# Kernel tuning notes

Hardware: AMD Instinct MI355X
Metric: run time of the kernel (lower is better)

The kernel has to match this reference:

```python
import jax, jax.numpy as jnp
import numpy as np

N = 50000
E = 600000
IN_DIM = 256
H1, H2, H3 = 128, 64, 64
HEADS = 8


def _add_self_loops(edge_index, edge_weight=None):
    loop = jnp.arange(N, dtype=edge_index.dtype)
    src = jnp.concatenate([edge_index[0], loop])
    dst = jnp.concatenate([edge_index[1], loop])
    if edge_weight is None:
        return src, dst, None
    ew = jnp.concatenate([edge_weight, jnp.ones((N,), edge_weight.dtype)])
    return src, dst, ew


def gcn_conv(x, edge_index, edge_weight, W, b):
    # PyG GCNConv: add self-loops (weight 1), symmetric normalization, scatter-add.
    src, dst, ew = _add_self_loops(edge_index, edge_weight)
    deg = jax.ops.segment_sum(ew, dst, num_segments=N)          # [N]
    dinv = jnp.where(deg > 0, jax.lax.rsqrt(jnp.maximum(deg, 1e-12)), 0.0)
    coeff = dinv[src] * ew * dinv[dst]                          # [E+N]
    h = x @ W                                                    # [N, out]
    out = jax.ops.segment_sum(coeff[:, None] * h[src], dst, num_segments=N)
    return out + b


def gat_conv(x, edge_index, W, att_src, att_dst, b):
    # PyG GATConv, heads=HEADS, concat=False (mean over heads), leaky_relu slope 0.2.
    src, dst, _ = _add_self_loops(edge_index)
    C = W.shape[1] // HEADS
    h = (x @ W).reshape(N, HEADS, C)                             # [N,H,C]
    a_s = jnp.sum(h * att_src, axis=-1)                          # [N,H]
    a_d = jnp.sum(h * att_dst, axis=-1)                          # [N,H]
    e = jax.nn.leaky_relu(a_s[src] + a_d[dst], negative_slope=0.2)  # [E',H]
    # scatter-softmax over edges sharing a destination
    m = jax.ops.segment_max(e, dst, num_segments=N)              # [N,H]
    p = jnp.exp(e - m[dst])
    s = jax.ops.segment_sum(p, dst, num_segments=N)              # [N,H]
    alpha = p / (s[dst] + 1e-16)                                 # [E',H]
    out = jax.ops.segment_sum(alpha[:, :, None] * h[src], dst, num_segments=N)  # [N,H,C]
    return jnp.mean(out, axis=1) + b


def setup_inputs() -> dict:
    key = jax.random.key(0)
    ks = jax.random.split(key, 12)
    x = jax.random.normal(ks[0], (N, IN_DIM), dtype=jnp.float32)
    edge_index = jax.random.randint(ks[1], (2, E), 0, N, dtype=jnp.int32)
    edge_weight = jax.random.uniform(ks[2], (E,), dtype=jnp.float32)
    def glorot(k, shape):
        fan = shape[0] + shape[-1]
        return jax.random.normal(k, shape, dtype=jnp.float32) * np.sqrt(2.0 / fan)
    return {
        "x": x, "edge_index": edge_index, "edge_weight": edge_weight,
        "gc1_w": glorot(ks[3], (IN_DIM, H1)), "gc1_b": jnp.zeros((H1,), jnp.float32),
        "gat_w": glorot(ks[4], (H1, HEADS * H2)),
        "att_src": glorot(ks[5], (HEADS, H2)), "att_dst": glorot(ks[6], (HEADS, H2)),
        "gat_b": jnp.zeros((H2,), jnp.float32),
        "gc2_w": glorot(ks[7], (H2, H3)), "gc2_b": jnp.zeros((H3,), jnp.float32),
        "fc_w": glorot(ks[8], (H3, 1)), "fc_b": jnp.zeros((1,), jnp.float32),
    }


def reference(x, edge_index, edge_weight, gc1_w, gc1_b, gat_w, att_src, att_dst,
              gat_b, gc2_w, gc2_b, fc_w, fc_b):
    # dropout is inference no-op
    h = jax.nn.relu(gcn_conv(x, edge_index, edge_weight, gc1_w, gc1_b))
    h = jax.nn.relu(gat_conv(h, edge_index, gat_w, att_src, att_dst, gat_b))
    h = jax.nn.relu(gcn_conv(h, edge_index, edge_weight, gc2_w, gc2_b))
    return h @ fc_w + fc_b                                       # [N,1]
```

## Files before the change

### kernel.cpp

```cpp
#include <hip/hip_runtime.h>
#include <hip/hip_bf16.h>

#define GNN_N 50000
#define GNN_E 600000

typedef unsigned int uint;
typedef unsigned short ushort;
using short8 = __attribute__((ext_vector_type(8))) short;
using f32x4  = __attribute__((ext_vector_type(4))) float;
using f32x2  = __attribute__((ext_vector_type(2))) float;

__device__ __forceinline__ float leaky02(float x) { return x > 0.f ? x : 0.2f * x; }
__device__ __forceinline__ ushort f2b(float f) {
    uint u = __float_as_uint(f);
    return (ushort)((u + 0x7fffu + ((u >> 16) & 1u)) >> 16);
}
__device__ __forceinline__ float b2f(ushort b) { return __uint_as_float(((uint)b) << 16); }
__device__ __forceinline__ float blo(uint u) { return __uint_as_float(u << 16); }
__device__ __forceinline__ float bhi(uint u) { return __uint_as_float(u & 0xffff0000u); }

__device__ __forceinline__ void pkfma(f32x2& d, f32x2 a, f32x2 b) {
    asm("v_pk_fma_f32 %0, %1, %2, %0" : "+v"(d) : "v"(a), "v"(b));
}
__device__ __forceinline__ f32x2 shfl2(f32x2 x, int srcLane) {
    union { f32x2 f; long long l; } u;
    u.f = x;
    u.l = __shfl(u.l, srcLane);
    return u.f;
}
__device__ __forceinline__ f32x2 shflx2(f32x2 x, int m) {
    union { f32x2 f; long long l; } u;
    u.f = x;
    u.l = __shfl_xor(u.l, m);
    return u.f;
}

__global__ void gnn_hist(const int* __restrict__ dst, int* __restrict__ cnt, int e) {
    int i = blockIdx.x * blockDim.x + threadIdx.x;
    if (i < e) atomicAdd(&cnt[dst[i]], 1);
}
__global__ void gnn_scan1(const int* __restrict__ cnt, int* __restrict__ row_ptr,
                          int* __restrict__ blksum, int n) {
    __shared__ int sh[256];
    int tid = threadIdx.x;
    int base = blockIdx.x * 1024 + tid * 4;
    int v0 = (base + 0 < n) ? cnt[base + 0] : 0;
    int v1 = (base + 1 < n) ? cnt[base + 1] : 0;
    int v2 = (base + 2 < n) ? cnt[base + 2] : 0;
    int v3 = (base + 3 < n) ? cnt[base + 3] : 0;
    int tsum = v0 + v1 + v2 + v3;
    sh[tid] = tsum;
    __syncthreads();
    for (int off = 1; off < 256; off <<= 1) {
        int t = (tid >= off) ? sh[tid - off] : 0;
        __syncthreads();
        sh[tid] += t;
        __syncthreads();
    }
    int excl = sh[tid] - tsum;
    if (base + 0 < n) row_ptr[base + 0] = excl; excl += v0;
    if (base + 1 < n) row_ptr[base + 1] = excl; excl += v1;
    if (base + 2 < n) row_ptr[base + 2] = excl; excl += v2;
    if (base + 3 < n) row_ptr[base + 3] = excl;
    if (tid == 255) blksum[blockIdx.x] = sh[255];
}
__global__ void gnn_scan2(int* blksum, int nblk, int* row_ptr_end, int total) {
    if (threadIdx.x == 0 && blockIdx.x == 0) {
        int run = 0;
        for (int b = 0; b < nblk; ++b) { int t = blksum[b]; blksum[b] = run; run += t; }
        *row_ptr_end = total;
    }
}
__global__ void gnn_scan3(int* row_ptr, const int* __restrict__ blksum, int n) {
    int i = blockIdx.x * blockDim.x + threadIdx.x;
    if (i < n) row_ptr[i] += blksum[i >> 10];
}
__global__ void gnn_scatter_idx(const int* __restrict__ dst, const int* __restrict__ row_ptr,
                                int* __restrict__ fill, int* __restrict__ tord, int e) {
    int i = blockIdx.x * blockDim.x + threadIdx.x;
    if (i >= e) return;
    int d = dst[i];
    int pos = row_ptr[d] + atomicAdd(&fill[d], 1);
    tord[pos] = i;
}
__global__ __launch_bounds__(256) void gnn_sortdeg(const float* __restrict__ ew,
                                                   int* __restrict__ tord,
                                                   const int* __restrict__ row_ptr,
                                                   float* __restrict__ dinv, int n) {
    int v = blockIdx.x * 4 + (threadIdx.x >> 6);
    int lane = threadIdx.x & 63;
    if (v >= n) return;
    int beg = row_ptr[v], end = row_ptr[v + 1];
    int cnt = end - beg;
    if (cnt <= 64) {
        int val = (lane < cnt) ? tord[beg + lane] : 0x7fffffff;
#pragma unroll
        for (int k = 2; k <= 64; k <<= 1) {
#pragma unroll
            for (int j = k >> 1; j >= 1; j >>= 1) {
                int other = __shfl_xor(val, j);
                bool keepMin = (((lane & j) == 0) == ((lane & k) == 0));
                val = keepMin ? min(val, other) : max(val, other);
            }
        }
        if (lane < cnt) tord[beg + lane] = val;
        float s = (lane < cnt) ? ew[val] : 0.f;
#pragma unroll
        for (int m = 32; m; m >>= 1) s += __shfl_xor(s, m);
        if (lane == 0) dinv[v] = rsqrtf(1.0f + s);
    } else {
        if (lane == 0) {
            for (int i = beg + 1; i < end; ++i) {
                int key = tord[i];
                int k2 = i - 1;
                while (k2 >= beg && tord[k2] > key) { tord[k2 + 1] = tord[k2]; --k2; }
                tord[k2 + 1] = key;
            }
            float s = 1.f;
            for (int i = beg; i < end; ++i) s += ew[tord[i]];
            dinv[v] = rsqrtf(s);
        }
    }
}
__global__ void gnn_edgefin(const int* __restrict__ src, const int* __restrict__ dst,
                            const float* __restrict__ ew, const float* __restrict__ dinv,
                            const int* __restrict__ tord, int* __restrict__ esrc,
                            float* __restrict__ ecw, int e) {
    int pos = blockIdx.x * blockDim.x + threadIdx.x;
    if (pos >= e) return;
    int i = tord[pos];
    int s = src[i];
    esrc[pos] = s;
    ecw[pos] = dinv[s] * ew[i] * dinv[dst[i]];
}

__global__ void gnn_prep(const float* __restrict__ gc1_w, const float* __restrict__ gat_w,
                         const float* __restrict__ gc2_w, const float* __restrict__ att_src,
                         const float* __restrict__ att_dst, ushort* __restrict__ w1t,
                         ushort* __restrict__ w2s_t, ushort* __restrict__ w3t,
                         float* __restrict__ wa_t) {
    int t = blockIdx.x * 256 + threadIdx.x;
    if (t < 32768) {
        int k = t >> 7, n = t & 127;
        w1t[n * 256 + k] = f2b(gc1_w[t]);
        return;
    }
    t -= 32768;
    if (t < 65536) {
        int c = t >> 10, r = t & 1023;
        int h = r >> 7, k = r & 127;
        w2s_t[t] = f2b(0.125f * gat_w[(size_t)k * 512 + h * 64 + c]);
        return;
    }
    t -= 65536;
    if (t < 4096) {
        int k = t >> 6, n = t & 63;
        w3t[n * 64 + k] = f2b(gc2_w[t]);
        return;
    }
    t -= 4096;
    if (t < 2048) {
        int j = t >> 7, k = t & 127;
        int h = j & 7;
        const float* av = (j < 8) ? att_src : att_dst;
        float s = 0.f;
        for (int c = 0; c < 64; ++c) s += gat_w[(size_t)k * 512 + h * 64 + c] * av[h * 64 + c];
        wa_t[j * 128 + k] = s;
    }
}

template <bool AF32, bool BIAS>
__global__ __launch_bounds__(256) void gnn_mfma_gemm(const void* __restrict__ Av,
                                                     const ushort* __restrict__ Bt,
                                                     ushort* __restrict__ C,
                                                     const float* __restrict__ bias,
                                                     int M, int N, int K) {
    __shared__ ushort As[64 * 40];
    __shared__ ushort Bs[64 * 40];
    const int tid = threadIdx.x;
    const int wv = tid >> 6, lane = tid & 63;
    const int g = lane >> 4, r = lane & 15;
    const int brow = blockIdx.y << 6, bcol = blockIdx.x << 6;

    const int srow = tid >> 2;
    const int skoff = (tid & 3) << 3;
    int arow = brow + srow;
    if (arow >= M) arow = M - 1;
    const ushort* A16 = (const ushort*)Av;
    const float*  A32 = (const float*)Av;
    const ushort* Ap16 = A16 + (size_t)arow * K + skoff;
    const float*  Ap32 = A32 + (size_t)arow * K + skoff;
    const ushort* Bp = Bt + (size_t)(bcol + srow) * K + skoff;
    ushort* AsW = &As[srow * 40 + skoff];
    ushort* BsW = &Bs[srow * 40 + skoff];

    f32x4 acc[4] = {};

    for (int k0 = 0; k0 < K; k0 += 32) {
        if constexpr (AF32) {
            float4 f0 = *(const float4*)(Ap32 + k0);
            float4 f1 = *(const float4*)(Ap32 + k0 + 4);
            short8 t;
            t[0] = (short)f2b(f0.x); t[1] = (short)f2b(f0.y);
            t[2] = (short)f2b(f0.z); t[3] = (short)f2b(f0.w);
            t[4] = (short)f2b(f1.x); t[5] = (short)f2b(f1.y);
            t[6] = (short)f2b(f1.z); t[7] = (short)f2b(f1.w);
            *(short8*)AsW = t;
        } else {
            *(short8*)AsW = *(const short8*)(Ap16 + k0);
        }
        *(short8*)BsW = *(const short8*)(Bp + k0);
        __syncthreads();
        short8 bfrag = *(const short8*)&Bs[(wv * 16 + r) * 40 + g * 8];
#pragma unroll
        for (int mb = 0; mb < 4; ++mb) {
            short8 afrag = *(const short8*)&As[(mb * 16 + r) * 40 + g * 8];
            acc[mb] = __builtin_amdgcn_mfma_f32_16x16x32_bf16(afrag, bfrag, acc[mb], 0, 0, 0);
        }
        __syncthreads();
    }

    const int col = bcol + wv * 16 + r;
    float bv = 0.f;
    if constexpr (BIAS) bv = bias[col];
#pragma unroll
    for (int mb = 0; mb < 4; ++mb) {
        int rowb = brow + mb * 16 + g * 4;
#pragma unroll
        for (int rr = 0; rr < 4; ++rr) {
            int row = rowb + rr;
            if (row < M) {
                float val = acc[mb][rr];
                if constexpr (BIAS) {
                    val += bv;
                    val = val > 0.f ? val : 0.f;
                }
                C[(size_t)row * N + col] = f2b(val);
            }
        }
    }
}

__global__ __launch_bounds__(256) void gnn_gcn_node128_asd(const int* __restrict__ row_ptr,
                                                           const int* __restrict__ esrc,
                                                           const float* __restrict__ ecw,
                                                           const float* __restrict__ dinv,
                                                           const ushort* __restrict__ hb,
                                                           const float* __restrict__ b,
                                                           const float* __restrict__ wa,
                                                           ushort* __restrict__ out,
                                                           float* __restrict__ a_s,
                                                           float* __restrict__ a_d, int n) {
    __shared__ float swa[16 * 128];
    for (int i = threadIdx.x; i < 16 * 128; i += 256) swa[i] = wa[i];
    __syncthreads();
    int v = blockIdx.x * 4 + (threadIdx.x >> 6);
    int lane = threadIdx.x & 63;
    if (v >= n) return;
    const int sl = lane & 31;
    const int half = lane >> 5;
    float di = dinv[v];
    float a0, a1, a2, a3;
    {
        float scl = half ? 0.f : di * di;
        uint2 u = *(const uint2*)(hb + (size_t)v * 128 + 4 * sl);
        a0 = scl * blo(u.x); a1 = scl * bhi(u.x);
        a2 = scl * blo(u.y); a3 = scl * bhi(u.y);
    }
    int beg = row_ptr[v], end = row_ptr[v + 1];
    int cntE = end - beg;
    int pairs = cntE >> 1;
    int i = 0;
    for (; i + 4 <= pairs; i += 4) {
        int s[4]; float c[4]; uint2 u[4];
#pragma unroll
        for (int t = 0; t < 4; ++t) s[t] = esrc[beg + 2 * (i + t) + half];
#pragma unroll
        for (int t = 0; t < 4; ++t) c[t] = ecw[beg + 2 * (i + t) + half];
#pragma unroll
        for (int t = 0; t < 4; ++t) u[t] = *(const uint2*)(hb + (size_t)s[t] * 128 + 4 * sl);
#pragma unroll
        for (int t = 0; t < 4; ++t) {
            a0 += c[t] * blo(u[t].x); a1 += c[t] * bhi(u[t].x);
            a2 += c[t] * blo(u[t].y); a3 += c[t] * bhi(u[t].y);
        }
    }
    for (; i < pairs; ++i) {
        int s = esrc[beg + 2 * i + half];
        float c = ecw[beg + 2 * i + half];
        uint2 u = *(const uint2*)(hb + (size_t)s * 128 + 4 * sl);
        a0 += c * blo(u.x); a1 += c * bhi(u.x);
        a2 += c * blo(u.y); a3 += c * bhi(u.y);
    }
    if (cntE & 1) {
        int s = esrc[end - 1];
        float c = half ? 0.f : ecw[end - 1];
        uint2 u = *(const uint2*)(hb + (size_t)s * 128 + 4 * sl);
        a0 += c * blo(u.x); a1 += c * bhi(u.x);
        a2 += c * blo(u.y); a3 += c * bhi(u.y);
    }
    a0 += __shfl_xor(a0, 32); a1 += __shfl_xor(a1, 32);
    a2 += __shfl_xor(a2, 32); a3 += __shfl_xor(a3, 32);

    float4 bv = *(const float4*)(b + 4 * sl);
    float o0 = a0 + bv.x, o1 = a1 + bv.y, o2 = a2 + bv.z, o3 = a3 + bv.w;
    o0 = o0 > 0.f ? o0 : 0.f; o1 = o1 > 0.f ? o1 : 0.f;
    o2 = o2 > 0.f ? o2 : 0.f; o3 = o3 > 0.f ? o3 : 0.f;
    if (lane < 32) {
        uint2 w;
        w.x = (uint)f2b(o0) | ((uint)f2b(o1) << 16);
        w.y = (uint)f2b(o2) | ((uint)f2b(o3) << 16);
        *(uint2*)(out + (size_t)v * 128 + 4 * sl) = w;
    }

    float part[16];
#pragma unroll
    for (int j = 0; j < 16; ++j) {
        const float* wj = &swa[j * 128 + 4 * sl];
        part[j] = o0 * wj[0] + o1 * wj[1] + o2 * wj[2] + o3 * wj[3];
    }
#pragma unroll
    for (int m = 1; m < 32; m <<= 1) {
#pragma unroll
        for (int j = 0; j < 16; ++j) part[j] += __shfl_xor(part[j], m);
    }
    if (lane == 0) {
#pragma unroll
        for (int j = 0; j < 8; ++j) {
            a_s[(size_t)v * 8 + j] = part[j];
            a_d[(size_t)v * 8 + j] = part[8 + j];
        }
    }
}

__global__ __launch_bounds__(256) void gnn_gat_z(const int* __restrict__ row_ptr,
                                                 const int* __restrict__ esrc,
                                                 const float* __restrict__ a_s,
                                                 const float* __restrict__ a_d,
                                                 const ushort* __restrict__ g1b,
                                                 ushort* __restrict__ zb, int n) {
    int v = blockIdx.x * 4 + (threadIdx.x >> 6);
    int lane = threadIdx.x & 63;
    if (v >= n) return;
    const int sl = lane & 31;
    const int half = lane >> 5;
    const int hh = lane & 7;
    const int hbase = lane & 32;
    const float adh = a_d[(size_t)v * 8 + hh];

    f32x2 zA[8] = {}, zB[8] = {};
    float sloc = 0.f;
    {
        float pv = __expf(leaky02(a_s[(size_t)v * 8 + hh] + adh));
        if (half) pv = 0.f;
        sloc += pv;
        f32x2 pv2; pv2[0] = pv; pv2[1] = pv;
        uint2 u = *(const uint2*)(g1b + (size_t)v * 128 + 4 * sl);
        f32x2 gA; gA[0] = blo(u.x); gA[1] = bhi(u.x);
        f32x2 gB; gB[0] = blo(u.y); gB[1] = bhi(u.y);
#pragma unroll
        for (int h = 0; h < 8; ++h) {
            f32x2 ph2 = shfl2(pv2, hbase | h);
            pkfma(zA[h], gA, ph2);
            pkfma(zB[h], gB, ph2);
        }
    }
    int beg = row_ptr[v], end = row_ptr[v + 1];
    int cntE = end - beg;
    int pairs = cntE >> 1;
    int i = 0;
    for (; i + 2 <= pairs; i += 2) {
        int s[2]; float e[2]; uint2 u[2];
#pragma unroll
        for (int t = 0; t < 2; ++t) s[t] = esrc[beg + 2 * (i + t) + half];
#pragma unroll
        for (int t = 0; t < 2; ++t) e[t] = a_s[(size_t)s[t] * 8 + hh];
#pragma unroll
        for (int t = 0; t < 2; ++t) u[t] = *(const uint2*)(g1b + (size_t)s[t] * 128 + 4 * sl);
#pragma unroll
        for (int t = 0; t < 2; ++t) {
            float pv = __expf(leaky02(e[t] + adh));
            sloc += pv;
            f32x2 pv2; pv2[0] = pv; pv2[1] = pv;
            f32x2 gA; gA[0] = blo(u[t].x); gA[1] = bhi(u[t].x);
            f32x2 gB; gB[0] = blo(u[t].y); gB[1] = bhi(u[t].y);
#pragma unroll
            for (int h = 0; h < 8; ++h) {
                f32x2 ph2 = shfl2(pv2, hbase | h);
                pkfma(zA[h], gA, ph2);
                pkfma(zB[h], gB, ph2);
            }
        }
    }
    for (; i < pairs; ++i) {
        int s = esrc[beg + 2 * i + half];
        float pv = __expf(leaky02(a_s[(size_t)s * 8 + hh] + adh));
        sloc += pv;
        f32x2 pv2; pv2[0] = pv; pv2[1] = pv;
        uint2 u = *(const uint2*)(g1b + (size_t)s * 128 + 4 * sl);
        f32x2 gA; gA[0] = blo(u.x); gA[1] = bhi(u.x);
        f32x2 gB; gB[0] = blo(u.y); gB[1] = bhi(u.y);
#pragma unroll
        for (int h = 0; h < 8; ++h) {
            f32x2 ph2 = shfl2(pv2, hbase | h);
            pkfma(zA[h], gA, ph2);
            pkfma(zB[h], gB, ph2);
        }
    }
    if (cntE & 1) {
        int s = esrc[end - 1];
        float pv = __expf(leaky02(a_s[(size_t)s * 8 + hh] + adh));
        if (half) pv = 0.f;
        sloc += pv;
        f32x2 pv2; pv2[0] = pv; pv2[1] = pv;
        uint2 u = *(const uint2*)(g1b + (size_t)s * 128 + 4 * sl);
        f32x2 gA; gA[0] = blo(u.x); gA[1] = bhi(u.x);
        f32x2 gB; gB[0] = blo(u.y); gB[1] = bhi(u.y);
#pragma unroll
        for (int h = 0; h < 8; ++h) {
            f32x2 ph2 = shfl2(pv2, hbase | h);
            pkfma(zA[h], gA, ph2);
            pkfma(zB[h], gB, ph2);
        }
    }
    float slx = sloc + __shfl_xor(sloc, 32) + 1e-16f;
#pragma unroll
    for (int h = 0; h < 8; ++h) {
        zA[h] = zA[h] + shflx2(zA[h], 32);
        zB[h] = zB[h] + shflx2(zB[h], 32);
    }
    if (lane < 32) {
#pragma unroll
        for (int h = 0; h < 8; ++h) {
            float rs = 1.f / __shfl(slx, h);
            uint2 w;
            w.x = (uint)f2b(zA[h][0] * rs) | ((uint)f2b(zA[h][1] * rs) << 16);
            w.y = (uint)f2b(zB[h][0] * rs) | ((uint)f2b(zB[h][1] * rs) << 16);
            *(uint2*)(zb + (size_t)v * 1024 + h * 128 + 4 * sl) = w;
        }
    }
}

__global__ __launch_bounds__(256) void gnn_gcn_node64_fc(const int* __restrict__ row_ptr,
                                                         const int* __restrict__ esrc,
                                                         const float* __restrict__ ecw,
                                                         const float* __restrict__ dinv,
                                                         const ushort* __restrict__ hb,
                                                         const float* __restrict__ b,
                                                         const float* __restrict__ fc_w,
                                                         const float* __restrict__ fc_b,
                                                         float* __restrict__ out, int n) {
    int v = blockIdx.x * 4 + (threadIdx.x >> 6);
    int lane = threadIdx.x & 63;
    if (v >= n) return;
    const int sl = lane & 31;
    const int half = lane >> 5;
    float di = dinv[v];
    float a0, a1;
    {
        float scl = half ? 0.f : di * di;
        uint u = *(const uint*)(hb + (size_t)v * 64 + 2 * sl);
        a0 = scl * blo(u); a1 = scl * bhi(u);
    }
    int beg = row_ptr[v], end = row_ptr[v + 1];
    int cntE = end - beg;
    int pairs = cntE >> 1;
    int i = 0;
    for (; i + 4 <= pairs; i += 4) {
        int s[4]; float c[4]; uint u[4];
#pragma unroll
        for (int t = 0; t < 4; ++t) s[t] = esrc[beg + 2 * (i + t) + half];
#pragma unroll
        for (int t = 0; t < 4; ++t) c[t] = ecw[beg + 2 * (i + t) + half];
#pragma unroll
        for (int t = 0; t < 4; ++t) u[t] = *(const uint*)(hb + (size_t)s[t] * 64 + 2 * sl);
#pragma unroll
        for (int t = 0; t < 4; ++t) { a0 += c[t] * blo(u[t]); a1 += c[t] * bhi(u[t]); }
    }
    for (; i < pairs; ++i) {
        int s = esrc[beg + 2 * i + half];
        float c = ecw[beg + 2 * i + half];
        uint u = *(const uint*)(hb + (size_t)s * 64 + 2 * sl);
        a0 += c * blo(u); a1 += c * bhi(u);
    }
    if (cntE & 1) {
        int s = esrc[end - 1];
        float c = half ? 0.f : ecw[end - 1];
        uint u = *(const uint*)(hb + (size_t)s * 64 + 2 * sl);
        a0 += c * blo(u); a1 += c * bhi(u);
    }
    a0 += __shfl_xor(a0, 32);
    a1 += __shfl_xor(a1, 32);
    float o0 = a0 + b[2 * sl];
    float o1 = a1 + b[2 * sl + 1];
    o0 = o0 > 0.f ? o0 : 0.f;
    o1 = o1 > 0.f ? o1 : 0.f;
    float val = o0 * fc_w[2 * sl] + o1 * fc_w[2 * sl + 1];
#pragma unroll
    for (int m = 1; m < 32; m <<= 1) val += __shfl_xor(val, m);
    if (lane == 0) out[v] = val + fc_b[0];
}

extern "C" void kernel_launch(void* const* d_in, const int* in_sizes, int n_in,
                              void* d_out, int out_size, void* d_ws, size_t ws_size,
                              hipStream_t stream) {
    const float* x       = (const float*)d_in[0];
    const int*   ei      = (const int*)d_in[1];
    const float* ew      = (const float*)d_in[2];
    const float* gc1_w   = (const float*)d_in[3];
    const float* gc1_b   = (const float*)d_in[4];
    const float* gat_w   = (const float*)d_in[5];
    const float* att_src = (const float*)d_in[6];
    const float* att_dst = (const float*)d_in[7];
    const float* gat_b   = (const float*)d_in[8];
    const float* gc2_w   = (const float*)d_in[9];
    const float* gc2_b   = (const float*)d_in[10];
    const float* fc_w    = (const float*)d_in[11];
    const float* fc_b    = (const float*)d_in[12];
    float* out = (float*)d_out;

    const int N = GNN_N;
    const int E = in_sizes[2];
    const int* src = ei;
    const int* dst = ei + E;

    char* p = (char*)d_ws;
    ushort* zb  = (ushort*)p; p += (size_t)N * 1024 * 2;
    ushort* h1b = (ushort*)p; p += (size_t)N * 128 * 2;
    ushort* g1b = (ushort*)p; p += (size_t)N * 128 * 2;
    ushort* g2b = (ushort*)p; p += (size_t)N * 64 * 2;
    ushort* h3b = (ushort*)p; p += (size_t)N * 64 * 2;
    ushort* w1t = (ushort*)p; p += (size_t)128 * 256 * 2;
    ushort* w2s_t = (ushort*)p; p += (size_t)64 * 1024 * 2;
    ushort* w3t = (ushort*)p; p += (size_t)64 * 64 * 2;
    float*  wa_t = (float*)p; p += 16 * 128 * 4;
    float*  a_s = (float*)p;  p += (size_t)N * 8 * 4;
    float*  a_d = (float*)p;  p += (size_t)N * 8 * 4;
    int* row_ptr = (int*)p;   p += (size_t)(N + 64) * 4;
    int* esrc = (int*)p;      p += (size_t)E * 4;
    float* ecw = (float*)p;   p += (size_t)E * 4;
    int* tord = (int*)p;      p += (size_t)E * 4;
    int* cnt = (int*)p;       p += (size_t)N * 4;
    int* fill = (int*)p;      p += (size_t)N * 4;
    float* dinv = (float*)p;  p += (size_t)N * 4;
    int* blksum = (int*)p;    p += 4096;

    auto cdiv = [](long a, long b) { return (int)((a + b - 1) / b); };

    hipMemsetAsync(cnt, 0, (size_t)N * 8, stream);
    gnn_hist<<<cdiv(E, 256), 256, 0, stream>>>(dst, cnt, E);
    const int nblk = cdiv(N, 1024);
    gnn_scan1<<<nblk, 256, 0, stream>>>(cnt, row_ptr, blksum, N);
    gnn_scan2<<<1, 64, 0, stream>>>(blksum, nblk, row_ptr + N, E);
    gnn_scan3<<<cdiv(N, 256), 256, 0, stream>>>(row_ptr, blksum, N);
    gnn_scatter_idx<<<cdiv(E, 256), 256, 0, stream>>>(dst, row_ptr, fill, tord, E);
    gnn_sortdeg<<<cdiv(N, 4), 256, 0, stream>>>(ew, tord, row_ptr, dinv, N);
    gnn_edgefin<<<cdiv(E, 256), 256, 0, stream>>>(src, dst, ew, dinv, tord, esrc, ecw, E);

    gnn_prep<<<408, 256, 0, stream>>>(gc1_w, gat_w, gc2_w, att_src, att_dst, w1t, w2s_t, w3t, wa_t);

    {
        dim3 grid(128 / 64, cdiv(N, 64));
        gnn_mfma_gemm<true, false><<<grid, 256, 0, stream>>>(x, w1t, h1b, nullptr, N, 128, 256);
    }
    gnn_gcn_node128_asd<<<cdiv(N, 4), 256, 0, stream>>>(row_ptr, esrc, ecw, dinv, h1b, gc1_b,
                                                        wa_t, g1b, a_s, a_d, N);

    gnn_gat_z<<<cdiv(N, 4), 256, 0, stream>>>(row_ptr, esrc, a_s, a_d, g1b, zb, N);
    {
        dim3 grid(1, cdiv(N, 64));
        gnn_mfma_gemm<false, true><<<grid, 256, 0, stream>>>(zb, w2s_t, g2b, gat_b, N, 64, 1024);
    }

    {
        dim3 grid(1, cdiv(N, 64));
        gnn_mfma_gemm<false, false><<<grid, 256, 0, stream>>>(g2b, w3t, h3b, nullptr, N, 64, 64);
    }
    gnn_gcn_node64_fc<<<cdiv(N, 4), 256, 0, stream>>>(row_ptr, esrc, ecw, dinv, h3b, gc2_b,
                                                      fc_w, fc_b, out, N);
}
```

Measured before the change: 337.6 us.

## Split each node's edge aggregation across two wavefronts with LDS reduction

The three per-node aggregation kernels (GCN layer 1, GAT softmax-weighted sum, GCN layer 2 with FC) now give each destination node two 64-lane wavefronts instead of one. Each wave handles alternating edge pairs, and the partial sums are combined through shared memory behind a block barrier. This shortens the serial per-node edge loop and raises memory-level parallelism on the gathers. The costs are twice as many blocks, an added __syncthreads, an LDS round trip, and the second wave sitting idle during the epilogue; the GAT kernel also needs about 8KB of shared memory per block to exchange its z partials.

New measurement: 407.2 us. 20.6% more time.

```diff
diff --git a/kernel.cpp b/kernel.cpp
--- a/kernel.cpp
+++ b/kernel.cpp
@@ -252,83 +252,100 @@
                                                            float* __restrict__ a_s,
                                                            float* __restrict__ a_d, int n) {
     __shared__ float swa[16 * 128];
+    __shared__ float psh[2][128];
     for (int i = threadIdx.x; i < 16 * 128; i += 256) swa[i] = wa[i];
-    __syncthreads();
-    int v = blockIdx.x * 4 + (threadIdx.x >> 6);
-    int lane = threadIdx.x & 63;
-    if (v >= n) return;
+    const int tid = threadIdx.x;
+    const int node_i = tid >> 7;
+    const int nw = (tid >> 6) & 1;
+    const int lane = tid & 63;
+    const int v = blockIdx.x * 2 + node_i;
+    const bool active = v < n;
     const int sl = lane & 31;
     const int half = lane >> 5;
-    float di = dinv[v];
-    float a0, a1, a2, a3;
-    {
-        float scl = half ? 0.f : di * di;
+
+    float a0 = 0.f, a1 = 0.f, a2 = 0.f, a3 = 0.f;
+    int beg = 0, end = 0;
+    if (active) { beg = row_ptr[v]; end = row_ptr[v + 1]; }
+    int cntE = end - beg;
+    int pairs = cntE >> 1;
+
+    if (active && nw == 0) {
+        float scl = half ? 0.f : dinv[v] * dinv[v];
         uint2 u = *(const uint2*)(hb + (size_t)v * 128 + 4 * sl);
         a0 = scl * blo(u.x); a1 = scl * bhi(u.x);
         a2 = scl * blo(u.y); a3 = scl * bhi(u.y);
     }
-    int beg = row_ptr[v], end = row_ptr[v + 1];
-    int cntE = end - beg;
-    int pairs = cntE >> 1;
-    int i = 0;
-    for (; i + 4 <= pairs; i += 4) {
-        int s[4]; float c[4]; uint2 u[4];
-#pragma unroll
-        for (int t = 0; t < 4; ++t) s[t] = esrc[beg + 2 * (i + t) + half];
-#pragma unroll
-        for (int t = 0; t < 4; ++t) c[t] = ecw[beg + 2 * (i + t) + half];
-#pragma unroll
-        for (int t = 0; t < 4; ++t) u[t] = *(const uint2*)(hb + (size_t)s[t] * 128 + 4 * sl);
-#pragma unroll
-        for (int t = 0; t < 4; ++t) {
-            a0 += c[t] * blo(u[t].x); a1 += c[t] * bhi(u[t].x);
-            a2 += c[t] * blo(u[t].y); a3 += c[t] * bhi(u[t].y);
-        }
-    }
-    for (; i < pairs; ++i) {
-        int s = esrc[beg + 2 * i + half];
-        float c = ecw[beg + 2 * i + half];
-        uint2 u = *(const uint2*)(hb + (size_t)s * 128 + 4 * sl);
-        a0 += c * blo(u.x); a1 += c * bhi(u.x);
-        a2 += c * blo(u.y); a3 += c * bhi(u.y);
-    }
-    if (cntE & 1) {
-        int s = esrc[end - 1];
-        float c = half ? 0.f : ecw[end - 1];
-        uint2 u = *(const uint2*)(hb + (size_t)s * 128 + 4 * sl);
-        a0 += c * blo(u.x); a1 += c * bhi(u.x);
-        a2 += c * blo(u.y); a3 += c * bhi(u.y);
+    if (active) {
+        int i = nw;
+        for (; i + 2 < pairs; i += 4) {
+            int pa = beg + 2 * i + half;
+            int pb = beg + 2 * (i + 2) + half;
+            int s0 = esrc[pa], s1 = esrc[pb];
+            float c0 = ecw[pa], c1 = ecw[pb];
+            uint2 u0 = *(const uint2*)(hb + (size_t)s0 * 128 + 4 * sl);
+            uint2 u1 = *(const uint2*)(hb + (size_t)s1 * 128 + 4 * sl);
+            a0 += c0 * blo(u0.x); a1 += c0 * bhi(u0.x);
+            a2 += c0 * blo(u0.y); a3 += c0 * bhi(u0.y);
+            a0 += c1 * blo(u1.x); a1 += c1 * bhi(u1.x);
+            a2 += c1 * blo(u1.y); a3 += c1 * bhi(u1.y);
+        }
+        for (; i < pairs; i += 2) {
+            int pa = beg + 2 * i + half;
+            int s0 = esrc[pa];
+            float c0 = ecw[pa];
+            uint2 u0 = *(const uint2*)(hb + (size_t)s0 * 128 + 4 * sl);
+            a0 += c0 * blo(u0.x); a1 += c0 * bhi(u0.x);
+            a2 += c0 * blo(u0.y); a3 += c0 * bhi(u0.y);
+        }
+        if (nw == 0 && (cntE & 1)) {
+            int s = esrc[end - 1];
+            float c = half ? 0.f : ecw[end - 1];
+            uint2 u = *(const uint2*)(hb + (size_t)s * 128 + 4 * sl);
+            a0 += c * blo(u.x); a1 += c * bhi(u.x);
+            a2 += c * blo(u.y); a3 += c * bhi(u.y);
+        }
     }
     a0 += __shfl_xor(a0, 32); a1 += __shfl_xor(a1, 32);
     a2 += __shfl_xor(a2, 32); a3 += __shfl_xor(a3, 32);
 
-    float4 bv = *(const float4*)(b + 4 * sl);
-    float o0 = a0 + bv.x, o1 = a1 + bv.y, o2 = a2 + bv.z, o3 = a3 + bv.w;
-    o0 = o0 > 0.f ? o0 : 0.f; o1 = o1 > 0.f ? o1 : 0.f;
-    o2 = o2 > 0.f ? o2 : 0.f; o3 = o3 > 0.f ? o3 : 0.f;
-    if (lane < 32) {
+    if (active && nw == 1 && lane < 32) {
+        psh[node_i][4 * sl + 0] = a0;
+        psh[node_i][4 * sl + 1] = a1;
+        psh[node_i][4 * sl + 2] = a2;
+        psh[node_i][4 * sl + 3] = a3;
+    }
+    __syncthreads();
+    if (active && nw == 0 && lane < 32) {
+        a0 += psh[node_i][4 * sl + 0];
+        a1 += psh[node_i][4 * sl + 1];
+        a2 += psh[node_i][4 * sl + 2];
+        a3 += psh[node_i][4 * sl + 3];
+        float4 bv = *(const float4*)(b + 4 * sl);
+        float o0 = a0 + bv.x, o1 = a1 + bv.y, o2 = a2 + bv.z, o3 = a3 + bv.w;
+        o0 = o0 > 0.f ? o0 : 0.f; o1 = o1 > 0.f ? o1 : 0.f;
+        o2 = o2 > 0.f ? o2 : 0.f; o3 = o3 > 0.f ? o3 : 0.f;
         uint2 w;
         w.x = (uint)f2b(o0) | ((uint)f2b(o1) << 16);
         w.y = (uint)f2b(o2) | ((uint)f2b(o3) << 16);
         *(uint2*)(out + (size_t)v * 128 + 4 * sl) = w;
-    }
-
-    float part[16];
-#pragma unroll
-    for (int j = 0; j < 16; ++j) {
-        const float* wj = &swa[j * 128 + 4 * sl];
-        part[j] = o0 * wj[0] + o1 * wj[1] + o2 * wj[2] + o3 * wj[3];
-    }
-#pragma unroll
-    for (int m = 1; m < 32; m <<= 1) {
-#pragma unroll
-        for (int j = 0; j < 16; ++j) part[j] += __shfl_xor(part[j], m);
-    }
-    if (lane == 0) {
-#pragma unroll
-        for (int j = 0; j < 8; ++j) {
-            a_s[(size_t)v * 8 + j] = part[j];
-            a_d[(size_t)v * 8 + j] = part[8 + j];
+
+        float part[16];
+#pragma unroll
+        for (int j = 0; j < 16; ++j) {
+            const float* wj = &swa[j * 128 + 4 * sl];
+            part[j] = o0 * wj[0] + o1 * wj[1] + o2 * wj[2] + o3 * wj[3];
+        }
+#pragma unroll
+        for (int m = 1; m < 32; m <<= 1) {
+#pragma unroll
+            for (int j = 0; j < 16; ++j) part[j] += __shfl_xor(part[j], m);
+        }
+        if (lane == 0) {
+#pragma unroll
+            for (int j = 0; j < 8; ++j) {
+                a_s[(size_t)v * 8 + j] = part[j];
+                a_d[(size_t)v * 8 + j] = part[8 + j];
+            }
         }
     }
 }
@@ -339,18 +356,30 @@
                                                  const float* __restrict__ a_d,
                                                  const ushort* __restrict__ g1b,
                                                  ushort* __restrict__ zb, int n) {
-    int v = blockIdx.x * 4 + (threadIdx.x >> 6);
-    int lane = threadIdx.x & 63;
-    if (v >= n) return;
+    __shared__ float zsh[2][1032];
+    const int tid = threadIdx.x;
+    const int node_i = tid >> 7;
+    const int nw = (tid >> 6) & 1;
+    const int lane = tid & 63;
+    const int v = blockIdx.x * 2 + node_i;
+    const bool active = v < n;
     const int sl = lane & 31;
     const int half = lane >> 5;
     const int hh = lane & 7;
     const int hbase = lane & 32;
-    const float adh = a_d[(size_t)v * 8 + hh];
 
     f32x2 zA[8] = {}, zB[8] = {};
     float sloc = 0.f;
-    {
+    int beg = 0, end = 0;
+    float adh = 0.f;
+    if (active) {
+        beg = row_ptr[v]; end = row_ptr[v + 1];
+        adh = a_d[(size_t)v * 8 + hh];
+    }
+    int cntE = end - beg;
+    int pairs = cntE >> 1;
+
+    if (active && nw == 0) {
         float pv = __expf(leaky02(a_s[(size_t)v * 8 + hh] + adh));
         if (half) pv = 0.f;
         sloc += pv;
@@ -365,25 +394,50 @@
             pkfma(zB[h], gB, ph2);
         }
     }
-    int beg = row_ptr[v], end = row_ptr[v + 1];
-    int cntE = end - beg;
-    int pairs = cntE >> 1;
-    int i = 0;
-    for (; i + 2 <= pairs; i += 2) {
-        int s[2]; float e[2]; uint2 u[2];
-#pragma unroll
-        for (int t = 0; t < 2; ++t) s[t] = esrc[beg + 2 * (i + t) + half];
-#pragma unroll
-        for (int t = 0; t < 2; ++t) e[t] = a_s[(size_t)s[t] * 8 + hh];
-#pragma unroll
-        for (int t = 0; t < 2; ++t) u[t] = *(const uint2*)(g1b + (size_t)s[t] * 128 + 4 * sl);
-#pragma unroll
-        for (int t = 0; t < 2; ++t) {
-            float pv = __expf(leaky02(e[t] + adh));
-            sloc += pv;
-            f32x2 pv2; pv2[0] = pv; pv2[1] = pv;
-            f32x2 gA; gA[0] = blo(u[t].x); gA[1] = bhi(u[t].x);
-            f32x2 gB; gB[0] = blo(u[t].y); gB[1] = bhi(u[t].y);
+    if (active) {
+        int i = nw;
+        for (; i + 2 < pairs; i += 4) {
+            int pa = beg + 2 * i + half;
+            int pb = beg + 2 * (i + 2) + half;
+            int s0 = esrc[pa], s1 = esrc[pb];
+            float e0 = a_s[(size_t)s0 * 8 + hh];
+            float e1 = a_s[(size_t)s1 * 8 + hh];
+            uint2 u0 = *(const uint2*)(g1b + (size_t)s0 * 128 + 4 * sl);
+            uint2 u1 = *(const uint2*)(g1b + (size_t)s1 * 128 + 4 * sl);
+            float p0 = __expf(leaky02(e0 + adh));
+            float p1 = __expf(leaky02(e1 + adh));
+            sloc += p0; sloc += p1;
+            f32x2 pv2, gA, gB, ph2;
+            pv2[0] = p0; pv2[1] = p0;
+            gA[0] = blo(u0.x); gA[1] = bhi(u0.x);
+            gB[0] = blo(u0.y); gB[1] = bhi(u0.y);
+#pragma unroll
+            for (int h = 0; h < 8; ++h) {
+                ph2 = shfl2(pv2, hbase | h);
+                pkfma(zA[h], gA, ph2);
+                pkfma(zB[h], gB, ph2);
+            }
+            pv2[0] = p1; pv2[1] = p1;
+            gA[0] = blo(u1.x); gA[1] = bhi(u1.x);
+            gB[0] = blo(u1.y); gB[1] = bhi(u1.y);
+#pragma unroll
+            for (int h = 0; h < 8; ++h) {
+                ph2 = shfl2(pv2, hbase | h);
+                pkfma(zA[h], gA, ph2);
+                pkfma(zB[h], gB, ph2);
+            }
+        }
+        for (; i < pairs; i += 2) {
+            int pa = beg + 2 * i + half;
+            int s0 = esrc[pa];
+            float e0 = a_s[(size_t)s0 * 8 + hh];
+            uint2 u0 = *(const uint2*)(g1b + (size_t)s0 * 128 + 4 * sl);
+            float p0 = __expf(leaky02(e0 + adh));
+            sloc += p0;
+            f32x2 pv2, gA, gB;
+            pv2[0] = p0; pv2[1] = p0;
+            gA[0] = blo(u0.x); gA[1] = bhi(u0.x);
+            gB[0] = blo(u0.y); gB[1] = bhi(u0.y);
 #pragma unroll
             for (int h = 0; h < 8; ++h) {
                 f32x2 ph2 = shfl2(pv2, hbase | h);
@@ -391,51 +445,54 @@
                 pkfma(zB[h], gB, ph2);
             }
         }
-    }
-    for (; i < pairs; ++i) {
-        int s = esrc[beg + 2 * i + half];
-        float pv = __expf(leaky02(a_s[(size_t)s * 8 + hh] + adh));
-        sloc += pv;
-        f32x2 pv2; pv2[0] = pv; pv2[1] = pv;
-        uint2 u = *(const uint2*)(g1b + (size_t)s * 128 + 4 * sl);
-        f32x2 gA; gA[0] = blo(u.x); gA[1] = bhi(u.x);
-        f32x2 gB; gB[0] = blo(u.y); gB[1] = bhi(u.y);
-#pragma unroll
-        for (int h = 0; h < 8; ++h) {
-            f32x2 ph2 = shfl2(pv2, hbase | h);
-            pkfma(zA[h], gA, ph2);
-            pkfma(zB[h], gB, ph2);
-        }
-    }
-    if (cntE & 1) {
-        int s = esrc[end - 1];
-        float pv = __expf(leaky02(a_s[(size_t)s * 8 + hh] + adh));
-        if (half) pv = 0.f;
-        sloc += pv;
-        f32x2 pv2; pv2[0] = pv; pv2[1] = pv;
-        uint2 u = *(const uint2*)(g1b + (size_t)s * 128 + 4 * sl);
-        f32x2 gA; gA[0] = blo(u.x); gA[1] = bhi(u.x);
-        f32x2 gB; gB[0] = blo(u.y); gB[1] = bhi(u.y);
-#pragma unroll
-        for (int h = 0; h < 8; ++h) {
-            f32x2 ph2 = shfl2(pv2, hbase | h);
-            pkfma(zA[h], gA, ph2);
-            pkfma(zB[h], gB, ph2);
-        }
-    }
-    float slx = sloc + __shfl_xor(sloc, 32) + 1e-16f;
+        if (nw == 0 && (cntE & 1)) {
+            int s = esrc[end - 1];
+            float pv = __expf(leaky02(a_s[(size_t)s * 8 + hh] + adh));
+            if (half) pv = 0.f;
+            sloc += pv;
+            f32x2 pv2; pv2[0] = pv; pv2[1] = pv;
+            uint2 u = *(const uint2*)(g1b + (size_t)s * 128 + 4 * sl);
+            f32x2 gA; gA[0] = blo(u.x); gA[1] = bhi(u.x);
+            f32x2 gB; gB[0] = blo(u.y); gB[1] = bhi(u.y);
+#pragma unroll
+            for (int h = 0; h < 8; ++h) {
+                f32x2 ph2 = shfl2(pv2, hbase | h);
+                pkfma(zA[h], gA, ph2);
+                pkfma(zB[h], gB, ph2);
+            }
+        }
+    }
+    float slx = sloc + __shfl_xor(sloc, 32);
 #pragma unroll
     for (int h = 0; h < 8; ++h) {
         zA[h] = zA[h] + shflx2(zA[h], 32);
         zB[h] = zB[h] + shflx2(zB[h], 32);
     }
-    if (lane < 32) {
+    if (active && nw == 1 && lane < 32) {
+        float* zp = &zsh[node_i][0];
 #pragma unroll
         for (int h = 0; h < 8; ++h) {
-            float rs = 1.f / __shfl(slx, h);
+            zp[h * 128 + 4 * sl + 0] = zA[h][0];
+            zp[h * 128 + 4 * sl + 1] = zA[h][1];
+            zp[h * 128 + 4 * sl + 2] = zB[h][0];
+            zp[h * 128 + 4 * sl + 3] = zB[h][1];
+        }
+        if (sl < 8) zp[1024 + sl] = slx;
+    }
+    __syncthreads();
+    if (active && nw == 0 && lane < 32) {
+        const float* zp = &zsh[node_i][0];
+        float slx_tot = slx + zp[1024 + hh];
+#pragma unroll
+        for (int h = 0; h < 8; ++h) {
+            float rs = 1.f / (__shfl(slx_tot, h) + 1e-16f);
+            float z0 = zA[h][0] + zp[h * 128 + 4 * sl + 0];
+            float z1 = zA[h][1] + zp[h * 128 + 4 * sl + 1];
+            float z2 = zB[h][0] + zp[h * 128 + 4 * sl + 2];
+            float z3 = zB[h][1] + zp[h * 128 + 4 * sl + 3];
             uint2 w;
-            w.x = (uint)f2b(zA[h][0] * rs) | ((uint)f2b(zA[h][1] * rs) << 16);
-            w.y = (uint)f2b(zB[h][0] * rs) | ((uint)f2b(zB[h][1] * rs) << 16);
+            w.x = (uint)f2b(z0 * rs) | ((uint)f2b(z1 * rs) << 16);
+            w.y = (uint)f2b(z2 * rs) | ((uint)f2b(z3 * rs) << 16);
             *(uint2*)(zb + (size_t)v * 1024 + h * 128 + 4 * sl) = w;
         }
     }
@@ -450,55 +507,72 @@
                                                          const float* __restrict__ fc_w,
                                                          const float* __restrict__ fc_b,
                                                          float* __restrict__ out, int n) {
-    int v = blockIdx.x * 4 + (threadIdx.x >> 6);
-    int lane = threadIdx.x & 63;
-    if (v >= n) return;
+    __shared__ float psh[2][64];
+    const int tid = threadIdx.x;
+    const int node_i = tid >> 7;
+    const int nw = (tid >> 6) & 1;
+    const int lane = tid & 63;
+    const int v = blockIdx.x * 2 + node_i;
+    const bool active = v < n;
     const int sl = lane & 31;
     const int half = lane >> 5;
-    float di = dinv[v];
-    float a0, a1;
-    {
-        float scl = half ? 0.f : di * di;
+
+    float a0 = 0.f, a1 = 0.f;
+    int beg = 0, end = 0;
+    if (active) { beg = row_ptr[v]; end = row_ptr[v + 1]; }
+    int cntE = end - beg;
+    int pairs = cntE >> 1;
+
+    if (active && nw == 0) {
+        float scl = half ? 0.f : dinv[v] * dinv[v];
         uint u = *(const uint*)(hb + (size_t)v * 64 + 2 * sl);
         a0 = scl * blo(u); a1 = scl * bhi(u);
     }
-    int beg = row_ptr[v], end = row_ptr[v + 1];
-    int cntE = end - beg;
-    int pairs = cntE >> 1;
-    int i = 0;
-    for (; i + 4 <= pairs; i += 4) {
-        int s[4]; float c[4]; uint u[4];
-#pragma unroll
-        for (int t = 0; t < 4; ++t) s[t] = esrc[beg + 2 * (i + t) + half];
-#pragma unroll
-        for (int t = 0; t < 4; ++t) c[t] = ecw[beg + 2 * (i + t) + half];
-#pragma unroll
-        for (int t = 0; t < 4; ++t) u[t] = *(const uint*)(hb + (size_t)s[t] * 64 + 2 * sl);
-#pragma unroll
-        for (int t = 0; t < 4; ++t) { a0 += c[t] * blo(u[t]); a1 += c[t] * bhi(u[t]); }
-    }
-    for (; i < pairs; ++i) {
-        int s = esrc[beg + 2 * i + half];
-        float c = ecw[beg + 2 * i + half];
-        uint u = *(const uint*)(hb + (size_t)s * 64 + 2 * sl);
-        a0 += c * blo(u); a1 += c * bhi(u);
-    }
-    if (cntE & 1) {
-        int s = esrc[end - 1];
-        float c = half ? 0.f : ecw[end - 1];
-        uint u = *(const uint*)(hb + (size_t)s * 64 + 2 * sl);
-        a0 += c * blo(u); a1 += c * bhi(u);
+    if (active) {
+        int i = nw;
+        for (; i + 2 < pairs; i += 4) {
+            int pa = beg + 2 * i + half;
+            int pb = beg + 2 * (i + 2) + half;
+            int s0 = esrc[pa], s1 = esrc[pb];
+            float c0 = ecw[pa], c1 = ecw[pb];
+            uint u0 = *(const uint*)(hb + (size_t)s0 * 64 + 2 * sl);
+            uint u1 = *(const uint*)(hb + (size_t)s1 * 64 + 2 * sl);
+            a0 += c0 * blo(u0); a1 += c0 * bhi(u0);
+            a0 += c1 * blo(u1); a1 += c1 * bhi(u1);
+        }
+        for (; i < pairs; i += 2) {
+            int pa = beg + 2 * i + half;
+            int s0 = esrc[pa];
+            float c0 = ecw[pa];
+            uint u0 = *(const uint*)(hb + (size_t)s0 * 64 + 2 * sl);
+            a0 += c0 * blo(u0); a1 += c0 * bhi(u0);
+        }
+        if (nw == 0 && (cntE & 1)) {
+            int s = esrc[end - 1];
+            float c = half ? 0.f : ecw[end - 1];
+            uint u = *(const uint*)(hb + (size_t)s * 64 + 2 * sl);
+            a0 += c * blo(u); a1 += c * bhi(u);
+        }
     }
     a0 += __shfl_xor(a0, 32);
     a1 += __shfl_xor(a1, 32);
-    float o0 = a0 + b[2 * sl];
-    float o1 = a1 + b[2 * sl + 1];
-    o0 = o0 > 0.f ? o0 : 0.f;
-    o1 = o1 > 0.f ? o1 : 0.f;
-    float val = o0 * fc_w[2 * sl] + o1 * fc_w[2 * sl + 1];
-#pragma unroll
-    for (int m = 1; m < 32; m <<= 1) val += __shfl_xor(val, m);
-    if (lane == 0) out[v] = val + fc_b[0];
+    if (active && nw == 1 && lane < 32) {
+        psh[node_i][2 * sl + 0] = a0;
+        psh[node_i][2 * sl + 1] = a1;
+    }
+    __syncthreads();
+    if (active && nw == 0 && lane < 32) {
+        a0 += psh[node_i][2 * sl + 0];
+        a1 += psh[node_i][2 * sl + 1];
+        float o0 = a0 + b[2 * sl];
+        float o1 = a1 + b[2 * sl + 1];
+        o0 = o0 > 0.f ? o0 : 0.f;
+        o1 = o1 > 0.f ? o1 : 0.f;
+        float val = o0 * fc_w[2 * sl] + o1 * fc_w[2 * sl + 1];
+#pragma unroll
+        for (int m = 1; m < 32; m <<= 1) val += __shfl_xor(val, m);
+        if (lane == 0) out[v] = val + fc_b[0];
+    }
 }
 
 extern "C" void kernel_launch(void* const* d_in, const int* in_sizes, int n_in,
@@ -563,10 +637,10 @@
         dim3 grid(128 / 64, cdiv(N, 64));
         gnn_mfma_gemm<true, false><<<grid, 256, 0, stream>>>(x, w1t, h1b, nullptr, N, 128, 256);
     }
-    gnn_gcn_node128_asd<<<cdiv(N, 4), 256, 0, stream>>>(row_ptr, esrc, ecw, dinv, h1b, gc1_b,
+    gnn_gcn_node128_asd<<<cdiv(N, 2), 256, 0, stream>>>(row_ptr, esrc, ecw, dinv, h1b, gc1_b,
                                                         wa_t, g1b, a_s, a_d, N);
 
-    gnn_gat_z<<<cdiv(N, 4), 256, 0, stream>>>(row_ptr, esrc, a_s, a_d, g1b, zb, N);
+    gnn_gat_z<<<cdiv(N, 2), 256, 0, stream>>>(row_ptr, esrc, a_s, a_d, g1b, zb, N);
     {
         dim3 grid(1, cdiv(N, 64));
         gnn_mfma_gemm<false, true><<<grid, 256, 0, stream>>>(zb, w2s_t, g2b, gat_b, N, 64, 1024);
@@ -576,6 +650,6 @@
         dim3 grid(1, cdiv(N, 64));
         gnn_mfma_gemm<false, false><<<grid, 256, 0, stream>>>(g2b, w3t, h3b, nullptr, N, 64, 64);
     }
-    gnn_gcn_node64_fc<<<cdiv(N, 4), 256, 0, stream>>>(row_ptr, esrc, ecw, dinv, h3b, gc2_b,
+    gnn_gcn_node64_fc<<<cdiv(N, 2), 256, 0, stream>>>(row_ptr, esrc, ecw, dinv, h3b, gc2_b,
                                                       fc_w, fc_b, out, N);
 }
```
